# Optimization experiments

Measured on AMD Instinct MI355X. Metric: run time of the kernel, lower is better.

The kernel has to match this reference:

```python
import jax, jax.numpy as jnp
import numpy as np

N, E, F_IN, H, C, G = 100000, 3200000, 256, 256, 10, 128
EPS = 1e-5


def _seg_sum(data, ids, n):
    return jax.ops.segment_sum(data, ids, num_segments=n)


def gcn_conv(x, W, b, src, dst, n):
    # PyG GCNConv: h = x @ W; add self-loops; sym-normalize by deg^{-1/2}; scatter-add; + bias
    h = x @ W  # [N, H]
    loop = jnp.arange(n)
    s = jnp.concatenate([src, loop])
    d = jnp.concatenate([dst, loop])
    deg = _seg_sum(jnp.ones(s.shape[0], dtype=h.dtype), d, n)  # in-degree incl. self-loop
    dis = jnp.where(deg > 0, jax.lax.rsqrt(deg), 0.0)
    norm = dis[s] * dis[d]  # [E+N]
    out = _seg_sum(h[s] * norm[:, None], d, n)  # gather -> scale -> scatter-add
    return out + b


def batch_norm(x, gamma, beta):
    # training-mode BN over the node/graph axis (biased variance, as torch)
    mean = jnp.mean(x, axis=0)
    var = jnp.var(x, axis=0)
    return (x - mean) * jax.lax.rsqrt(var + EPS) * gamma + beta


def setup_inputs() -> dict:
    key = jax.random.key(0)
    ks = jax.random.split(key, 16)
    inp = {
        "x": jax.random.normal(ks[0], (N, F_IN), dtype=jnp.float32),
        "edge_index": jax.random.randint(ks[1], (2, E), 0, N, dtype=jnp.int64)
        if jax.config.jax_enable_x64 else jax.random.randint(ks[1], (2, E), 0, N, dtype=jnp.int32),
        "batch": jnp.sort(jax.random.randint(ks[2], (N,), 0, G)),
    }
    dims_in = [F_IN, H, H]
    for i in range(3):
        scale = 1.0 / np.sqrt(dims_in[i])
        inp[f"W{i}"] = jax.random.normal(ks[3 + i], (dims_in[i], H), dtype=jnp.float32) * scale
        inp[f"b{i}"] = jnp.zeros((H,), dtype=jnp.float32)
        inp[f"g{i}"] = jnp.ones((H,), dtype=jnp.float32)
        inp[f"be{i}"] = jnp.zeros((H,), dtype=jnp.float32)
    inp["lin1_w"] = jax.random.normal(ks[8], (H, H), dtype=jnp.float32) / np.sqrt(H)
    inp["lin1_b"] = jnp.zeros((H,), dtype=jnp.float32)
    inp["bn1_g"] = jnp.ones((H,), dtype=jnp.float32)
    inp["bn1_b"] = jnp.zeros((H,), dtype=jnp.float32)
    inp["lin2_w"] = jax.random.normal(ks[9], (H, C), dtype=jnp.float32) / np.sqrt(H)
    inp["lin2_b"] = jnp.zeros((C,), dtype=jnp.float32)
    return inp


def reference(x, edge_index, batch,
              W0, b0, g0, be0, W1, b1, g1, be1, W2, b2, g2, be2,
              lin1_w, lin1_b, bn1_g, bn1_b, lin2_w, lin2_b):
    src, dst = edge_index[0], edge_index[1]
    Ws = [(W0, b0, g0, be0), (W1, b1, g1, be1), (W2, b2, g2, be2)]
    h = x
    for (W, b, g, be) in Ws:
        h = jax.nn.relu(batch_norm(gcn_conv(h, W, b, src, dst, N), g, be))
    # global mean pool over graphs
    sums = _seg_sum(h, batch, G)                                  # [G, H]
    cnt = _seg_sum(jnp.ones((N,), dtype=h.dtype), batch, G)       # [G]
    pooled = sums / jnp.maximum(cnt, 1.0)[:, None]
    z = jax.nn.relu(batch_norm(pooled @ lin1_w + lin1_b, bn1_g, bn1_b))
    # dropout is identity in eval mode
    return z @ lin2_w + lin2_b  # [G, C]
```

## Files before the change

### kernel.cpp

```cpp
#include <hip/hip_runtime.h>

#define N_NODES 100000
#define N_EDGES 3200000
#define HD      256
#define NGRAPH  128
#define NCLASS  10
#define BN_EPS  1e-5f
#define NBKT    782
#define NBLK    256
#define EPB     12500

typedef unsigned short u16;
typedef unsigned int   u32;
typedef __attribute__((ext_vector_type(4))) float f32x4;
typedef __attribute__((ext_vector_type(8))) float f32x8;
typedef __attribute__((ext_vector_type(8))) short bf16x8;
typedef __attribute__((ext_vector_type(8))) u16   u16x8;
typedef __attribute__((ext_vector_type(4))) u16   u16x4;

__device__ __forceinline__ float b2f(u16 u){ return __uint_as_float(((unsigned)u) << 16); }
__device__ __forceinline__ u16 f2b(float f){
  unsigned x = __float_as_uint(f);
  x += 0x7fffu + ((x >> 16) & 1u);
  return (u16)(x >> 16);
}
__device__ __forceinline__ f32x4 c4(u16x4 v){
  f32x4 r = { b2f(v[0]), b2f(v[1]), b2f(v[2]), b2f(v[3]) };
  return r;
}
__device__ __forceinline__ f32x8 c8(u16x8 v){
  f32x8 r = { b2f(v[0]), b2f(v[1]), b2f(v[2]), b2f(v[3]),
              b2f(v[4]), b2f(v[5]), b2f(v[6]), b2f(v[7]) };
  return r;
}


__global__ __launch_bounds__(256) void cvt_k(const float* __restrict__ x, u16* __restrict__ xb){
  size_t i = ((size_t)blockIdx.x * 256 + threadIdx.x) * 8;
  f32x4 v0 = *(const f32x4*)(x + i);
  f32x4 v1 = *(const f32x4*)(x + i + 4);
  u16x8 o = { f2b(v0[0]), f2b(v0[1]), f2b(v0[2]), f2b(v0[3]),
              f2b(v1[0]), f2b(v1[1]), f2b(v1[2]), f2b(v1[3]) };
  *(u16x8*)(xb + i) = o;
}

__global__ __launch_bounds__(256) void wt3_k(const float* __restrict__ W0, const float* __restrict__ W1,
                                             const float* __restrict__ W2, u16* __restrict__ Wt){
  int l = blockIdx.x >> 8;
  const float* W = (l == 0) ? W0 : (l == 1) ? W1 : W2;
  int i = (blockIdx.x & 255) * 256 + threadIdx.x;
  int k = i >> 8, n = i & 255;
  Wt[(size_t)l * HD * HD + n * HD + k] = f2b(W[k * HD + n]);
}

__global__ __launch_bounds__(256) void histA_k(const int* __restrict__ ei, u32* __restrict__ blkcnt){
  __shared__ u32 h[NBKT];
  int tid = threadIdx.x, blk = blockIdx.x;
  for (int j = tid; j < NBKT; j += 256) h[j] = 0;
  __syncthreads();
  const int* dst = ei + N_EDGES + blk * EPB;
  for (int i = tid; i < EPB; i += 256)
    atomicAdd(&h[((u32)dst[i]) >> 7], 1u);
  __syncthreads();
  for (int j = tid; j < NBKT; j += 256) blkcnt[blk * NBKT + j] = h[j];
}

__global__ __launch_bounds__(256) void scanB1_k(const u32* __restrict__ blkcnt, u32* __restrict__ offs_p,
                                                u32* __restrict__ total){
  __shared__ u32 sh[256];
  int b = blockIdx.x, tid = threadIdx.x;
  u32 v = blkcnt[tid * NBKT + b];
  sh[tid] = v;
  __syncthreads();
  #pragma unroll
  for (int o = 1; o < 256; o <<= 1){
    u32 t = (tid >= o) ? sh[tid - o] : 0u;
    __syncthreads();
    sh[tid] += t;
    __syncthreads();
  }
  offs_p[tid * NBKT + b] = sh[tid] - v;
  if (tid == 255) total[b] = sh[255];
}

__global__ __launch_bounds__(1024) void scanB2_k(const u32* __restrict__ total, u32* __restrict__ bkt_start){
  __shared__ u32 sh[1024];
  int tid = threadIdx.x;
  u32 v = (tid < NBKT) ? total[tid] : 0u;
  sh[tid] = v;
  __syncthreads();
  for (int o = 1; o < 1024; o <<= 1){
    u32 t = (tid >= o) ? sh[tid - o] : 0u;
    __syncthreads();
    sh[tid] += t;
    __syncthreads();
  }
  if (tid < NBKT) bkt_start[tid] = sh[tid] - v;
  if (tid == NBKT - 1) bkt_start[NBKT] = sh[tid];
}

__global__ __launch_bounds__(256) void scatC_k(const int* __restrict__ ei, const u32* __restrict__ offs_p,
                                               const u32* __restrict__ bkt_start,
                                               int* __restrict__ esrc, int* __restrict__ edst){
  __shared__ u32 base[NBKT];
  int tid = threadIdx.x, blk = blockIdx.x;
  for (int j = tid; j < NBKT; j += 256)
    base[j] = bkt_start[j] + offs_p[blk * NBKT + j];
  __syncthreads();
  const int* src = ei + blk * EPB;
  const int* dst = ei + N_EDGES + blk * EPB;
  for (int i = tid; i < EPB; i += 256){
    int s = src[i], d = dst[i];
    u32 pos = atomicAdd(&base[((u32)d) >> 7], 1u);
    esrc[pos] = s;
    edst[pos] = d;
  }
}

__global__ __launch_bounds__(128) void csrD_k(const int* __restrict__ esrc, const int* __restrict__ edst,
                                              const u32* __restrict__ bkt_start, int* __restrict__ rowptr,
                                              float* __restrict__ dis, int* __restrict__ colx){
  __shared__ u32 cnt[128], sc[128], bas[128];
  int b = blockIdx.x, tid = threadIdx.x;
  int seg0 = (int)bkt_start[b], seg1 = (int)bkt_start[b + 1];
  cnt[tid] = 0;
  __syncthreads();
  for (int i = seg0 + tid; i < seg1; i += 128)
    atomicAdd(&cnt[edst[i] & 127], 1u);
  __syncthreads();
  u32 mycnt = cnt[tid];
  sc[tid] = mycnt;
  __syncthreads();
  #pragma unroll
  for (int o = 1; o < 128; o <<= 1){
    u32 t = (tid >= o) ? sc[tid - o] : 0u;
    __syncthreads();
    sc[tid] += t;
    __syncthreads();
  }
  u32 excl = sc[tid] - mycnt;
  int node = (b << 7) + tid;
  bas[tid] = seg0 + excl;
  if (node <= N_NODES) rowptr[node] = seg0 + (int)excl;
  if (node < N_NODES) dis[node] = rsqrtf((float)(mycnt + 1));
  __syncthreads();
  cnt[tid] = 0;
  __syncthreads();
  for (int i = seg0 + tid; i < seg1; i += 128){
    int dl = edst[i] & 127;
    u32 p = atomicAdd(&cnt[dl], 1u);
    colx[bas[dl] + p] = esrc[i];
  }
}


__device__ __forceinline__ int swzoff(int row, int kel){
  return (row * 512 + kel * 2) ^ ((row & 7) << 4);
}

__global__ __launch_bounds__(256) void gemm_k(const u16* __restrict__ X, const u16* __restrict__ Wt,
                                              const float* __restrict__ dis, const float* __restrict__ prm,
                                              int useprm, u16* __restrict__ HN)
{
  __shared__ u16x8 AsV[2048];
  __shared__ u16x8 BsV[2048];
  char* As = (char*)AsV;
  char* Bs = (char*)BsV;
  int tid = threadIdx.x;
  int rowbase = blockIdx.x * 64;
  int r = tid >> 2, q = tid & 3;
  {
    int grow = rowbase + r;
    const u16* src = X + (size_t)grow * HD + q * 64;
    #pragma unroll
    for (int j = 0; j < 8; ++j){
      u16x8 v = {0,0,0,0,0,0,0,0};
      if (grow < N_NODES) v = *(const u16x8*)(src + j * 8);
      if (useprm){
        f32x8 a = *(const f32x8*)(prm + q * 64 + j * 8);
        f32x8 b = *(const f32x8*)(prm + HD + q * 64 + j * 8);
        f32x8 y = c8(v) * a + b;
        #pragma unroll
        for (int t = 0; t < 8; ++t) v[t] = f2b(fmaxf(y[t], 0.f));
      }
      *(u16x8*)(As + swzoff(r, q * 64 + j * 8)) = v;
    }
  }
  {
    const u16* wsrc = Wt + (size_t)r * HD + q * 64;
    #pragma unroll
    for (int j = 0; j < 8; ++j)
      *(u16x8*)(Bs + swzoff(r, q * 64 + j * 8)) = *(const u16x8*)(wsrc + j * 8);
  }
  __syncthreads();

  int w = tid >> 6, lane = tid & 63;
  int wm = w >> 1, wn = w & 1;
  int lr = lane & 15, lg = lane >> 4;

  u16x8 bR[8];

  #pragma unroll 1
  for (int panel = 0; panel < 4; ++panel){
    int colbase = panel * 64;
    if (panel < 3){
      const u16* wsrc = Wt + (size_t)(colbase + 64 + r) * HD + q * 64;
      #pragma unroll
      for (int j = 0; j < 8; ++j) bR[j] = *(const u16x8*)(wsrc + j * 8);
    }

    f32x4 acc00 = {0,0,0,0}, acc01 = {0,0,0,0}, acc10 = {0,0,0,0}, acc11 = {0,0,0,0};
    #pragma unroll
    for (int ks = 0; ks < 8; ++ks){
      int ka = ks * 32 + lg * 8;
      bf16x8 a0 = *(const bf16x8*)(As + swzoff(wm * 32 + lr,      ka));
      bf16x8 a1 = *(const bf16x8*)(As + swzoff(wm * 32 + 16 + lr, ka));
      bf16x8 b0 = *(const bf16x8*)(Bs + swzoff(wn * 32 + lr,      ka));
      bf16x8 b1 = *(const bf16x8*)(Bs + swzoff(wn * 32 + 16 + lr, ka));
      acc00 = __builtin_amdgcn_mfma_f32_16x16x32_bf16(a0, b0, acc00, 0, 0, 0);
      acc01 = __builtin_amdgcn_mfma_f32_16x16x32_bf16(a0, b1, acc01, 0, 0, 0);
      acc10 = __builtin_amdgcn_mfma_f32_16x16x32_bf16(a1, b0, acc10, 0, 0, 0);
      acc11 = __builtin_amdgcn_mfma_f32_16x16x32_bf16(a1, b1, acc11, 0, 0, 0);
    }

    #pragma unroll
    for (int mt = 0; mt < 2; ++mt){
      f32x4 ac0 = mt ? acc10 : acc00;
      f32x4 ac1 = mt ? acc11 : acc01;
      #pragma unroll
      for (int rr = 0; rr < 4; ++rr){
        int grow = rowbase + wm * 32 + mt * 16 + lg * 4 + rr;
        if (grow < N_NODES){
          float dd = dis[grow];
          size_t base = (size_t)grow * HD + colbase + wn * 32 + lr;
          HN[base]      = f2b(ac0[rr] * dd);
          HN[base + 16] = f2b(ac1[rr] * dd);
        }
      }
    }
    __syncthreads();
    if (panel < 3){
      #pragma unroll
      for (int j = 0; j < 8; ++j)
        *(u16x8*)(Bs + swzoff(r, q * 64 + j * 8)) = bR[j];
    }
    __syncthreads();
  }
}


__global__ __launch_bounds__(256) void agg_k(const u16* __restrict__ HN, const int* __restrict__ rowptr,
                                             const int* __restrict__ colx, const float* __restrict__ dis,
                                             u16* __restrict__ OUTB)
{
  int wid = threadIdx.x >> 6, lane = threadIdx.x & 63;
  int node = blockIdx.x * 8 + wid * 2 + (lane >> 5);
  int c0 = (lane & 31) * 8;
  const u16* base = HN + (size_t)c0;

  f32x8 a0 = {0,0,0,0,0,0,0,0}, a1 = a0, a2 = a0, a3 = a0;
  int e = rowptr[node], end = rowptr[node + 1];
  for (; e + 4 <= end; e += 4){
    int s0 = colx[e], s1 = colx[e + 1], s2 = colx[e + 2], s3 = colx[e + 3];
    u16x8 v0 = *(const u16x8*)(base + (size_t)s0 * HD);
    u16x8 v1 = *(const u16x8*)(base + (size_t)s1 * HD);
    u16x8 v2 = *(const u16x8*)(base + (size_t)s2 * HD);
    u16x8 v3 = *(const u16x8*)(base + (size_t)s3 * HD);
    a0 += c8(v0); a1 += c8(v1); a2 += c8(v2); a3 += c8(v3);
  }
  for (; e < end; ++e)
    a0 += c8(*(const u16x8*)(base + (size_t)colx[e] * HD));
  a0 += c8(*(const u16x8*)(base + (size_t)node * HD));
  f32x8 res = ((a0 + a1) + (a2 + a3)) * dis[node];
  u16x8 o = { f2b(res[0]), f2b(res[1]), f2b(res[2]), f2b(res[3]),
              f2b(res[4]), f2b(res[5]), f2b(res[6]), f2b(res[7]) };
  *(u16x8*)(OUTB + (size_t)node * HD + c0) = o;
}


__global__ __launch_bounds__(256) void stat1_k(const u16* __restrict__ OUTB, float* __restrict__ part){
  __shared__ float red[8][512];
  int tid = threadIdx.x;
  int c0 = (tid & 31) * 8;
  int rg = tid >> 5;
  f32x8 s = {0,0,0,0,0,0,0,0}, q = s;
  for (int r = blockIdx.x * 8 + rg; r < N_NODES; r += gridDim.x * 8){
    f32x8 v = c8(*(const u16x8*)(OUTB + (size_t)r * HD + c0));
    s += v; q += v * v;
  }
  #pragma unroll
  for (int e = 0; e < 8; ++e){
    red[rg][c0 + e] = s[e];
    red[rg][256 + c0 + e] = q[e];
  }
  __syncthreads();
  for (int slot = tid; slot < 512; slot += 256){
    float t = 0.f;
    #pragma unroll
    for (int g = 0; g < 8; ++g) t += red[g][slot];
    part[(size_t)blockIdx.x * 512 + slot] = t;
  }
}

__global__ __launch_bounds__(256) void stat2p_k(const float* __restrict__ part,
                                                const float* __restrict__ gamma,
                                                const float* __restrict__ beta,
                                                float* __restrict__ prm, int nblk){
  __shared__ float shs[256], shq[256];
  int c = blockIdx.x, tid = threadIdx.x;
  float s = 0.f, q = 0.f;
  for (int b = tid; b < nblk; b += 256){
    s += part[(size_t)b * 512 + c];
    q += part[(size_t)b * 512 + 256 + c];
  }
  shs[tid] = s; shq[tid] = q;
  __syncthreads();
  #pragma unroll
  for (int o = 128; o > 0; o >>= 1){
    if (tid < o){ shs[tid] += shs[tid + o]; shq[tid] += shq[tid + o]; }
    __syncthreads();
  }
  if (tid == 0){
    float mean = shs[0] / (float)N_NODES;
    float var  = fmaxf(shq[0] / (float)N_NODES - mean * mean, 0.f);
    float inv  = rsqrtf(var + BN_EPS);
    float a = gamma[c] * inv;
    prm[c] = a;
    prm[HD + c] = beta[c] - mean * a;
  }
}


__global__ __launch_bounds__(256) void bnd2_k(const int* __restrict__ batch, int* __restrict__ gs,
                                              int* __restrict__ ge){
  int i = blockIdx.x * 256 + threadIdx.x;
  if (i >= N_NODES) return;
  int b = batch[i];
  if (i == 0) gs[b] = 0;
  else {
    int p = batch[i - 1];
    if (p != b){ ge[p] = i; gs[b] = i; }
  }
  if (i == N_NODES - 1) ge[b] = N_NODES;
}

__global__ __launch_bounds__(256) void pool_k(const u16* __restrict__ outb, const float* __restrict__ prm,
                                              const int* __restrict__ gs, const int* __restrict__ ge,
                                              float* __restrict__ pooled){
  __shared__ float red[4][HD];
  int g = blockIdx.x;
  int s = gs[g], e = ge[g];
  int w = threadIdx.x >> 6;
  int c0 = (threadIdx.x & 63) * 4;
  f32x4 pa = *(const f32x4*)(prm + c0);
  f32x4 pb = *(const f32x4*)(prm + HD + c0);
  f32x4 acc = {0,0,0,0};
  for (int r = s + w; r < e; r += 4){
    f32x4 v = c4(*(const u16x4*)(outb + (size_t)r * HD + c0));
    f32x4 y = v * pa + pb;
    y[0] = fmaxf(y[0], 0.f); y[1] = fmaxf(y[1], 0.f);
    y[2] = fmaxf(y[2], 0.f); y[3] = fmaxf(y[3], 0.f);
    acc += y;
  }
  *(f32x4*)&red[w][c0] = acc;
  __syncthreads();
  if (w == 0){
    f32x4 t = *(f32x4*)&red[0][c0];
    t += *(f32x4*)&red[1][c0];
    t += *(f32x4*)&red[2][c0];
    t += *(f32x4*)&red[3][c0];
    float cntf = (e > s) ? (float)(e - s) : 1.0f;
    *(f32x4*)(pooled + g * HD + c0) = t * (1.0f / cntf);
  }
}

__global__ __launch_bounds__(256) void lin1_k(const float* __restrict__ pooled, const float* __restrict__ w,
                                              const float* __restrict__ b, float* __restrict__ z1){
  __shared__ float pr[HD];
  int g = blockIdx.x, c = threadIdx.x;
  pr[c] = pooled[g * HD + c];
  __syncthreads();
  float acc = b[c];
  #pragma unroll 8
  for (int k = 0; k < HD; ++k) acc = fmaf(pr[k], w[k * HD + c], acc);
  z1[g * HD + c] = acc;
}

__global__ __launch_bounds__(256) void bn1_k(float* __restrict__ z1, const float* __restrict__ g,
                                             const float* __restrict__ b){
  int c = threadIdx.x;
  float s = 0.f, q = 0.f;
  for (int r = 0; r < NGRAPH; ++r){
    float v = z1[r * HD + c];
    s += v; q += v * v;
  }
  float mean = s / (float)NGRAPH;
  float var  = fmaxf(q / (float)NGRAPH - mean * mean, 0.f);
  float inv  = rsqrtf(var + BN_EPS);
  float a = g[c] * inv, sh = b[c] - mean * a;
  for (int r = 0; r < NGRAPH; ++r)
    z1[r * HD + c] = fmaxf(z1[r * HD + c] * a + sh, 0.f);
}

__global__ __launch_bounds__(256) void lin2_k(const float* __restrict__ z1, const float* __restrict__ w,
                                              const float* __restrict__ b, float* __restrict__ out){
  __shared__ float zr[HD];
  int g = blockIdx.x;
  zr[threadIdx.x] = z1[g * HD + threadIdx.x];
  __syncthreads();
  if (threadIdx.x < NCLASS){
    float acc = b[threadIdx.x];
    #pragma unroll 8
    for (int k = 0; k < HD; ++k) acc = fmaf(zr[k], w[k * NCLASS + threadIdx.x], acc);
    out[g * NCLASS + threadIdx.x] = acc;
  }
}


extern "C" void kernel_launch(void* const* d_in, const int* in_sizes, int n_in,
                              void* d_out, int out_size, void* d_ws, size_t ws_size,
                              hipStream_t stream)
{
  const float* x      = (const float*)d_in[0];
  const int*   ei     = (const int*)d_in[1];
  const int*   batch  = (const int*)d_in[2];
  const float* W[3]   = {(const float*)d_in[3], (const float*)d_in[7], (const float*)d_in[11]};
  const float* gam[3] = {(const float*)d_in[5], (const float*)d_in[9], (const float*)d_in[13]};
  const float* bet[3] = {(const float*)d_in[6], (const float*)d_in[10], (const float*)d_in[14]};
  const float* lin1_w = (const float*)d_in[15];
  const float* lin1_b = (const float*)d_in[16];
  const float* bn1_g  = (const float*)d_in[17];
  const float* bn1_b  = (const float*)d_in[18];
  const float* lin2_w = (const float*)d_in[19];
  const float* lin2_b = (const float*)d_in[20];
  float* out = (float*)d_out;

  char* ws = (char*)d_ws;
  size_t off = 0;
  auto alloc = [&](size_t bytes) -> void* {
    void* p = ws + off;
    off = (off + bytes + 255) & ~(size_t)255;
    return p;
  };
  u16*   xb     = (u16*)alloc((size_t)N_NODES * HD * 2);
  u16*   hn     = (u16*)alloc((size_t)N_NODES * HD * 2);
  u16*   outb   = (u16*)alloc((size_t)N_NODES * HD * 2);
  u16*   wt     = (u16*)alloc((size_t)3 * HD * HD * 2);
  int*   rowptr = (int*)alloc((size_t)(N_NODES + 1) * 4);
  int*   colx   = (int*)alloc((size_t)N_EDGES * 4);
  float* dis    = (float*)alloc((size_t)N_NODES * 4);
  float* prm    = (float*)alloc(2 * HD * 4);
  float* part   = (float*)alloc((size_t)1024 * 512 * 4);
  int*   gs     = (int*)alloc(NGRAPH * 4);
  int*   ge     = (int*)alloc(NGRAPH * 4);
  float* pooled = (float*)alloc((size_t)NGRAPH * HD * 4);
  float* z1     = (float*)alloc((size_t)NGRAPH * HD * 4);
  (void)ws_size; (void)n_in; (void)in_sizes; (void)out_size;

  int* esrc      = (int*)outb;
  int* edst      = esrc + (size_t)N_EDGES;
  u32* blkcnt    = (u32*)(edst + (size_t)N_EDGES);
  u32* offs_p    = blkcnt + (size_t)NBLK * NBKT;
  u32* total     = (u32*)hn;
  u32* bkt_start = (u32*)hn + 1024;

  const int NB1 = (N_NODES + 255) / 256;

  cvt_k<<<12500, 256, 0, stream>>>(x, xb);
  wt3_k<<<768, 256, 0, stream>>>(W[0], W[1], W[2], wt);

  histA_k <<<NBLK, 256, 0, stream>>>(ei, blkcnt);
  scanB1_k<<<NBKT, 256, 0, stream>>>(blkcnt, offs_p, total);
  scanB2_k<<<1, 1024, 0, stream>>>(total, bkt_start);
  scatC_k <<<NBLK, 256, 0, stream>>>(ei, offs_p, bkt_start, esrc, edst);
  csrD_k  <<<NBKT, 128, 0, stream>>>(esrc, edst, bkt_start, rowptr, dis, colx);

  for (int l = 0; l < 3; ++l){
    const u16* gin = (l == 0) ? xb : outb;
    gemm_k<<<1563, 256, 0, stream>>>(gin, wt + (size_t)l * HD * HD, dis, prm, l > 0, hn);
    agg_k<<<12500, 256, 0, stream>>>(hn, rowptr, colx, dis, outb);
    stat1_k<<<1024, 256, 0, stream>>>(outb, part);
    stat2p_k<<<256, 256, 0, stream>>>(part, gam[l], bet[l], prm, 1024);
  }

  hipMemsetAsync(gs, 0x7f, NGRAPH * 4, stream);
  hipMemsetAsync(ge, 0, NGRAPH * 4, stream);
  bnd2_k<<<NB1, 256, 0, stream>>>(batch, gs, ge);
  pool_k<<<NGRAPH, 256, 0, stream>>>(outb, prm, gs, ge, pooled);
  lin1_k<<<NGRAPH, 256, 0, stream>>>(pooled, lin1_w, lin1_b, z1);
  bn1_k<<<1, 256, 0, stream>>>(z1, bn1_g, bn1_b);
  lin2_k<<<NGRAPH, 256, 0, stream>>>(z1, lin2_w, lin2_b, out);
}
```

Measured before the change: 1.262 ms.

## Fuse fp32-to-bf16 conversion into GEMM load and BN stats into aggregation

The standalone input conversion kernel is removed; the first-layer GEMM now reads fp32 x directly and converts to bf16 while staging into shared memory. The BN statistics pass is folded into the aggregation kernel, which reduces per-block sums and squares from fp32 results and writes per-block partials. This avoids a full 100k×256 read of the aggregated output per layer and an extra write/read of the bf16 input. In exchange, stat2p must now reduce 12500 partial rows instead of 1024, and the partial buffer grows considerably. The statistics also now come from the fp32 values before bf16 rounding.

```diff
diff --git a/kernel.cpp b/kernel.cpp
--- a/kernel.cpp
+++ b/kernel.cpp
@@ -9,6 +9,7 @@
 #define NBKT    782
 #define NBLK    256
 #define EPB     12500
+#define AGG_NB  12500
 
 typedef unsigned short u16;
 typedef unsigned int   u32;
@@ -34,16 +35,6 @@
   return r;
 }
 
-
-__global__ __launch_bounds__(256) void cvt_k(const float* __restrict__ x, u16* __restrict__ xb){
-  size_t i = ((size_t)blockIdx.x * 256 + threadIdx.x) * 8;
-  f32x4 v0 = *(const f32x4*)(x + i);
-  f32x4 v1 = *(const f32x4*)(x + i + 4);
-  u16x8 o = { f2b(v0[0]), f2b(v0[1]), f2b(v0[2]), f2b(v0[3]),
-              f2b(v1[0]), f2b(v1[1]), f2b(v1[2]), f2b(v1[3]) };
-  *(u16x8*)(xb + i) = o;
-}
-
 __global__ __launch_bounds__(256) void wt3_k(const float* __restrict__ W0, const float* __restrict__ W1,
                                              const float* __restrict__ W2, u16* __restrict__ Wt){
   int l = blockIdx.x >> 8;
@@ -158,7 +149,8 @@
   return (row * 512 + kel * 2) ^ ((row & 7) << 4);
 }
 
-__global__ __launch_bounds__(256) void gemm_k(const u16* __restrict__ X, const u16* __restrict__ Wt,
+__global__ __launch_bounds__(256) void gemm_k(const void* __restrict__ Xv, int xf32,
+                                              const u16* __restrict__ Wt,
                                               const float* __restrict__ dis, const float* __restrict__ prm,
                                               int useprm, u16* __restrict__ HN)
 {
@@ -171,17 +163,26 @@
   int r = tid >> 2, q = tid & 3;
   {
     int grow = rowbase + r;
-    const u16* src = X + (size_t)grow * HD + q * 64;
     #pragma unroll
     for (int j = 0; j < 8; ++j){
       u16x8 v = {0,0,0,0,0,0,0,0};
-      if (grow < N_NODES) v = *(const u16x8*)(src + j * 8);
-      if (useprm){
-        f32x8 a = *(const f32x8*)(prm + q * 64 + j * 8);
-        f32x8 b = *(const f32x8*)(prm + HD + q * 64 + j * 8);
-        f32x8 y = c8(v) * a + b;
-        #pragma unroll
-        for (int t = 0; t < 8; ++t) v[t] = f2b(fmaxf(y[t], 0.f));
+      if (grow < N_NODES){
+        if (xf32){
+          const float* src = (const float*)Xv + (size_t)grow * HD + q * 64 + j * 8;
+          f32x4 f0 = *(const f32x4*)src;
+          f32x4 f1 = *(const f32x4*)(src + 4);
+          v[0]=f2b(f0[0]); v[1]=f2b(f0[1]); v[2]=f2b(f0[2]); v[3]=f2b(f0[3]);
+          v[4]=f2b(f1[0]); v[5]=f2b(f1[1]); v[6]=f2b(f1[2]); v[7]=f2b(f1[3]);
+        } else {
+          v = *(const u16x8*)((const u16*)Xv + (size_t)grow * HD + q * 64 + j * 8);
+          if (useprm){
+            f32x8 a = *(const f32x8*)(prm + q * 64 + j * 8);
+            f32x8 b = *(const f32x8*)(prm + HD + q * 64 + j * 8);
+            f32x8 y = c8(v) * a + b;
+            #pragma unroll
+            for (int t = 0; t < 8; ++t) v[t] = f2b(fmaxf(y[t], 0.f));
+          }
+        }
       }
       *(u16x8*)(As + swzoff(r, q * 64 + j * 8)) = v;
     }
@@ -251,8 +252,9 @@
 
 __global__ __launch_bounds__(256) void agg_k(const u16* __restrict__ HN, const int* __restrict__ rowptr,
                                              const int* __restrict__ colx, const float* __restrict__ dis,
-                                             u16* __restrict__ OUTB)
+                                             u16* __restrict__ OUTB, float* __restrict__ part)
 {
+  __shared__ float red[8][512];
   int wid = threadIdx.x >> 6, lane = threadIdx.x & 63;
   int node = blockIdx.x * 8 + wid * 2 + (lane >> 5);
   int c0 = (lane & 31) * 8;
@@ -275,26 +277,15 @@
   u16x8 o = { f2b(res[0]), f2b(res[1]), f2b(res[2]), f2b(res[3]),
               f2b(res[4]), f2b(res[5]), f2b(res[6]), f2b(res[7]) };
   *(u16x8*)(OUTB + (size_t)node * HD + c0) = o;
-}
-
-
-__global__ __launch_bounds__(256) void stat1_k(const u16* __restrict__ OUTB, float* __restrict__ part){
-  __shared__ float red[8][512];
-  int tid = threadIdx.x;
-  int c0 = (tid & 31) * 8;
-  int rg = tid >> 5;
-  f32x8 s = {0,0,0,0,0,0,0,0}, q = s;
-  for (int r = blockIdx.x * 8 + rg; r < N_NODES; r += gridDim.x * 8){
-    f32x8 v = c8(*(const u16x8*)(OUTB + (size_t)r * HD + c0));
-    s += v; q += v * v;
-  }
+
+  int grp = wid * 2 + (lane >> 5);
   #pragma unroll
-  for (int e = 0; e < 8; ++e){
-    red[rg][c0 + e] = s[e];
-    red[rg][256 + c0 + e] = q[e];
-  }
-  __syncthreads();
-  for (int slot = tid; slot < 512; slot += 256){
+  for (int t = 0; t < 8; ++t){
+    red[grp][c0 + t] = res[t];
+    red[grp][256 + c0 + t] = res[t] * res[t];
+  }
+  __syncthreads();
+  for (int slot = threadIdx.x; slot < 512; slot += 256){
     float t = 0.f;
     #pragma unroll
     for (int g = 0; g < 8; ++g) t += red[g][slot];
@@ -442,7 +433,6 @@
     off = (off + bytes + 255) & ~(size_t)255;
     return p;
   };
-  u16*   xb     = (u16*)alloc((size_t)N_NODES * HD * 2);
   u16*   hn     = (u16*)alloc((size_t)N_NODES * HD * 2);
   u16*   outb   = (u16*)alloc((size_t)N_NODES * HD * 2);
   u16*   wt     = (u16*)alloc((size_t)3 * HD * HD * 2);
@@ -450,7 +440,7 @@
   int*   colx   = (int*)alloc((size_t)N_EDGES * 4);
   float* dis    = (float*)alloc((size_t)N_NODES * 4);
   float* prm    = (float*)alloc(2 * HD * 4);
-  float* part   = (float*)alloc((size_t)1024 * 512 * 4);
+  float* part   = (float*)alloc((size_t)AGG_NB * 512 * 4);
   int*   gs     = (int*)alloc(NGRAPH * 4);
   int*   ge     = (int*)alloc(NGRAPH * 4);
   float* pooled = (float*)alloc((size_t)NGRAPH * HD * 4);
@@ -466,7 +456,6 @@
 
   const int NB1 = (N_NODES + 255) / 256;
 
-  cvt_k<<<12500, 256, 0, stream>>>(x, xb);
   wt3_k<<<768, 256, 0, stream>>>(W[0], W[1], W[2], wt);
 
   histA_k <<<NBLK, 256, 0, stream>>>(ei, blkcnt);
@@ -476,11 +465,10 @@
   csrD_k  <<<NBKT, 128, 0, stream>>>(esrc, edst, bkt_start, rowptr, dis, colx);
 
   for (int l = 0; l < 3; ++l){
-    const u16* gin = (l == 0) ? xb : outb;
-    gemm_k<<<1563, 256, 0, stream>>>(gin, wt + (size_t)l * HD * HD, dis, prm, l > 0, hn);
-    agg_k<<<12500, 256, 0, stream>>>(hn, rowptr, colx, dis, outb);
-    stat1_k<<<1024, 256, 0, stream>>>(outb, part);
-    stat2p_k<<<256, 256, 0, stream>>>(part, gam[l], bet[l], prm, 1024);
+    const void* gin = (l == 0) ? (const void*)x : (const void*)outb;
+    gemm_k<<<1563, 256, 0, stream>>>(gin, l == 0, wt + (size_t)l * HD * HD, dis, prm, l > 0, hn);
+    agg_k<<<AGG_NB, 256, 0, stream>>>(hn, rowptr, colx, dis, outb, part);
+    stat2p_k<<<256, 256, 0, stream>>>(part, gam[l], bet[l], prm, AGG_NB);
   }
 
   hipMemsetAsync(gs, 0x7f, NGRAPH * 4, stream);
```

Result: slower. 1.343 ms (+6.4%).
